# Optimization experiments

Hardware: AMD Instinct MI355X
Metric: run time of the kernel (lower is better)

Reference implementation:

```python
import jax, jax.numpy as jnp
import numpy as np
from functools import partial

B, S, D_IN, H = 8, 2048, 1024, 1024
V = 50257
NUM_CODEWORDS, EMB_DIM = 256, 16
NUM_NEURONS, TOP_K = 64, 16  # top_k = sparsity(0.25) * 64
TILE_ROWS = 16
NUM_TILES = H // TILE_ROWS  # 64 -> decoder out_features = 1024
FREQS = (1.0, 2.0, 4.0)
MAX_LEN = 1024


def setup_inputs() -> dict:
    key = jax.random.key(0)
    ks = jax.random.split(key, 16)
    s = 0.02
    return {
        "inputs": jax.random.normal(ks[0], (B, S, D_IN), jnp.float32),
        "Wt": jax.random.normal(ks[1], (H, D_IN), jnp.float32) * s,
        "bt": jnp.zeros((H,), jnp.float32),
        "Wq": jax.random.normal(ks[2], (H, H), jnp.float32) * s,
        "bq": jnp.zeros((H,), jnp.float32),
        "Wk": jax.random.normal(ks[3], (H, H), jnp.float32) * s,
        "bk": jnp.zeros((H,), jnp.float32),
        "Wv": jax.random.normal(ks[4], (H, H), jnp.float32) * s,
        "bv": jnp.zeros((H,), jnp.float32),
        "Wo": jax.random.normal(ks[5], (D_IN, H), jnp.float32) * s,
        "bo": jnp.zeros((D_IN,), jnp.float32),
        "codebook": jax.random.normal(ks[6], (NUM_CODEWORDS, EMB_DIM), jnp.float32) * s,
        "instructions": jax.random.randint(ks[7], (NUM_TILES * TILE_ROWS, D_IN // EMB_DIM), 0, NUM_CODEWORDS),
        "W_lm": jax.random.normal(ks[8], (V, NUM_TILES * TILE_ROWS), jnp.float32) * s,
        "b_lm": jnp.zeros((V,), jnp.float32),
    }


def _positional_bias(seq_len):
    # AttentionBasisSynthesizer: sin/cos atoms at freqs (1,2,4), gains=1, shifts=0
    ang = 2.0 * jnp.pi * jnp.arange(seq_len, dtype=jnp.float32) / MAX_LEN
    bias = jnp.zeros((seq_len,), jnp.float32)
    for f in FREQS:
        bias = bias + jnp.sin(f * ang) + jnp.cos(f * ang)
    return bias  # [S]


def _forward(inputs, Wt, bt, Wq, bq, Wk, bk, Wv, bv, Wo, bo, codebook, instructions, W_lm, b_lm):
    tokens = inputs @ Wt.T + bt                       # [B,S,H]
    q = tokens @ Wq.T + bq
    k = tokens @ Wk.T + bk
    v = tokens @ Wv.T + bv
    # per-step KV-cache loop == causal attention over prefix; vectorize
    scores = jnp.einsum("bqh,bkh->bqk", q, k) / jnp.sqrt(jnp.float32(H))
    scores = scores + _positional_bias(S)[None, None, :]
    i = jnp.arange(S)
    causal = i[:, None] >= i[None, :]                 # [S,S]
    scores = jnp.where(causal[None], scores, -jnp.inf)
    attn = jnp.einsum("bqk,bkh->bqh", jax.nn.softmax(scores, axis=-1), v)  # [B,S,H]
    # sparse routing: group into NUM_NEURONS neurons, keep top-k by L2 norm,
    # softmax weights over kept neurons, straight-through combine with dense path
    g = attn.reshape(B, S, NUM_NEURONS, H // NUM_NEURONS)
    sc = jnp.sqrt(jnp.sum(g * g, axis=-1))            # [B,S,N]
    vals, idx = jax.lax.top_k(sc, TOP_K)              # [B,S,K]
    w = jax.nn.softmax(vals, axis=-1)
    onehot = jax.nn.one_hot(idx, NUM_NEURONS, dtype=attn.dtype)  # [B,S,K,N]
    wfull = jnp.einsum("bsk,bskn->bsn", w, onehot)    # [B,S,N]
    combined = (g * wfull[..., None]).reshape(B, S, H)
    combined = combined + (attn - jax.lax.stop_gradient(attn))  # straight-through
    dec_in = combined @ Wo.T + bo                     # [B,S,D_IN]
    x = jnp.mean(dec_in, axis=1)                      # [B,D_IN]
    # DemopackDecoder: weight rows assembled from codebook via instruction indices
    W_dec = codebook[instructions].reshape(NUM_TILES * TILE_ROWS, D_IN)
    hidden = x @ W_dec.T                              # [B, 1024]
    return hidden @ W_lm.T + b_lm                     # [B, V]


def reference(inputs, Wt, bt, Wq, bq, Wk, bk, Wv, bv, Wo, bo, codebook, instructions, W_lm, b_lm):
    return _forward(inputs, Wt, bt, Wq, bq, Wk, bk, Wv, bv, Wo, bo, codebook, instructions, W_lm, b_lm)
```

## Files before the change

### kernel.cpp

```cpp
#include <hip/hip_runtime.h>
#include <cstdint>
#include <cstddef>

#define B_   8
#define S_   2048
#define DIN_ 1024
#define H_   1024
#define V_   50257

typedef unsigned short ushort_t;
typedef __bf16 bf16x8 __attribute__((ext_vector_type(8)));
typedef float  f32x4  __attribute__((ext_vector_type(4)));

__device__ __forceinline__ ushort_t f2bf(float x) {
    unsigned u = __float_as_uint(x);
    u = (u + 0x7fffu + ((u >> 16) & 1u)) >> 16;
    return (ushort_t)u;
}

__device__ __forceinline__ void async16(const void* g, void* s) {
    __builtin_amdgcn_global_load_lds(
        (const __attribute__((address_space(1))) unsigned int*)g,
        (__attribute__((address_space(3))) unsigned int*)s, 16, 0, 0);
}

__device__ __forceinline__ float wredmax(float v) {
#pragma unroll
    for (int o = 32; o; o >>= 1) v = fmaxf(v, __shfl_xor(v, o));
    return v;
}
__device__ __forceinline__ float wredsum(float v) {
#pragma unroll
    for (int o = 32; o; o >>= 1) v += __shfl_xor(v, o);
    return v;
}

__global__ void f2bf_vec(const float* __restrict__ in, ushort_t* __restrict__ out, int n4) {
    int i = blockIdx.x * 256 + threadIdx.x;
    if (i >= n4) return;
    float4 f = ((const float4*)in)[i];
    ushort4 u;
    u.x = f2bf(f.x); u.y = f2bf(f.y); u.z = f2bf(f.z); u.w = f2bf(f.w);
    ((ushort4*)out)[i] = u;
}

__global__ void f2bf_w3(const float* __restrict__ Wq, const float* __restrict__ Wk,
                        const float* __restrict__ Wv, ushort_t* __restrict__ out) {
    int i = blockIdx.x * 256 + threadIdx.x;
    int w = i >> 18, off = i & 262143;
    const float* src = w == 0 ? Wq : (w == 1 ? Wk : Wv);
    float4 f = ((const float4*)src)[off];
    ushort4 u;
    u.x = f2bf(f.x); u.y = f2bf(f.y); u.z = f2bf(f.z); u.w = f2bf(f.w);
    ((ushort4*)(out + (size_t)w * 1048576))[off] = u;
}

__global__ void pos_bias_kernel(float* __restrict__ bias) {
    int k = blockIdx.x * 256 + threadIdx.x;
    if (k >= S_) return;
    float ang = 6.283185307179586f * (float)k / 1024.0f;
    float b = 0.f;
    b += sinf(1.f * ang) + cosf(1.f * ang);
    b += sinf(2.f * ang) + cosf(2.f * ang);
    b += sinf(4.f * ang) + cosf(4.f * ang);
    bias[k] = b;
}

__global__ __launch_bounds__(256)
void transpose_wt(const float* __restrict__ Wt, ushort_t* __restrict__ wtT) {
    __shared__ float t[64][65];
    int k0 = blockIdx.x * 64, i0 = blockIdx.y * 64;
    int tx = threadIdx.x & 63, ty = threadIdx.x >> 6;
#pragma unroll
    for (int j = 0; j < 16; j++) {
        int k = ty * 16 + j;
        t[k][tx] = Wt[(size_t)(k0 + k) * DIN_ + i0 + tx];
    }
    __syncthreads();
#pragma unroll
    for (int j = 0; j < 16; j++) {
        int i = ty * 16 + j;
        wtT[(size_t)(i0 + i) * H_ + k0 + tx] = f2bf(t[tx][i]);
    }
}

__global__ __launch_bounds__(256)
void bcomb_kernel(const float* __restrict__ Wq, const float* __restrict__ Wk,
                  const float* __restrict__ Wv, const float* __restrict__ bq,
                  const float* __restrict__ bk, const float* __restrict__ bv,
                  const float* __restrict__ bt, float* __restrict__ bcomb) {
    int wave = threadIdx.x >> 6, lane = threadIdx.x & 63;
    int j = blockIdx.x * 4 + wave;
    const float* W  = j < 1024 ? Wq : (j < 2048 ? Wk : Wv);
    const float* bb = j < 1024 ? bq : (j < 2048 ? bk : bv);
    int rowj = j & 1023;
    const float4* wr4 = (const float4*)(W + (size_t)rowj * 1024);
    const float4* bt4 = (const float4*)bt;
    float s = 0.f;
#pragma unroll
    for (int c = 0; c < 4; c++) {
        float4 w = wr4[c * 64 + lane];
        float4 b = bt4[c * 64 + lane];
        s += w.x * b.x + w.y * b.y + w.z * b.z + w.w * b.w;
    }
    s = wredsum(s);
    if (lane == 0) bcomb[j] = s + bb[rowj];
}

template <int OUT_BF16>
__global__ __launch_bounds__(256)
void gemm_bt(const ushort_t* __restrict__ A, int lda,
             const ushort_t* __restrict__ Bt, int ldb,
             void* __restrict__ Cv, int ldc, int K, const float* __restrict__ bias) {
    int bn = blockIdx.x, bm = blockIdx.y;
    __shared__ ushort_t As[128 * 32];
    __shared__ ushort_t Bs[128 * 32];
    int tid = threadIdx.x, wave = tid >> 6, lane = tid & 63;
    int wr = wave >> 1, wc = wave & 1;
    int nkt = K >> 5;
    int srow = lane >> 2, scol = (lane & 3) * 8;
    size_t arow0 = (size_t)bm * 128, brow0 = (size_t)bn * 128;
    f32x4 acc[4][4];
#pragma unroll
    for (int m = 0; m < 4; m++)
#pragma unroll
        for (int n = 0; n < 4; n++) acc[m][n] = f32x4{0.f, 0.f, 0.f, 0.f};
    for (int kt = 0; kt < nkt; ++kt) {
        int k0 = kt * 32;
#pragma unroll
        for (int i = 0; i < 2; i++) {
            int reg = wave * 2 + i;
            int row = reg * 16 + srow;
            async16(A + (arow0 + row) * (size_t)lda + k0 + scol, (ushort_t*)As + reg * 512);
            async16(Bt + (brow0 + row) * (size_t)ldb + k0 + scol, (ushort_t*)Bs + reg * 512);
        }
        __syncthreads();
        bf16x8 af[4], bfr[4];
#pragma unroll
        for (int m = 0; m < 4; m++)
            af[m] = *(const bf16x8*)&As[(wr * 64 + m * 16 + (lane & 15)) * 32 + (lane >> 4) * 8];
#pragma unroll
        for (int n = 0; n < 4; n++)
            bfr[n] = *(const bf16x8*)&Bs[(wc * 64 + n * 16 + (lane & 15)) * 32 + (lane >> 4) * 8];
#pragma unroll
        for (int m = 0; m < 4; m++)
#pragma unroll
            for (int n = 0; n < 4; n++)
                acc[m][n] = __builtin_amdgcn_mfma_f32_16x16x32_bf16(af[m], bfr[n], acc[m][n], 0, 0, 0);
        __syncthreads();
    }
    int rl = (lane >> 4) * 4, cl = lane & 15;
#pragma unroll
    for (int m = 0; m < 4; m++)
#pragma unroll
        for (int n = 0; n < 4; n++) {
            int col = bn * 128 + wc * 64 + n * 16 + cl;
            float badd = bias ? bias[col] : 0.f;
#pragma unroll
            for (int r = 0; r < 4; r++) {
                int row = bm * 128 + wr * 64 + m * 16 + rl + r;
                float v = acc[m][n][r] + badd;
                size_t off = (size_t)row * ldc + col;
                if (OUT_BF16) ((ushort_t*)Cv)[off] = f2bf(v);
                else          ((float*)Cv)[off] = v;
            }
        }
}

template <int OUT_BF16, int MODE>
__global__ __launch_bounds__(512, 2)
void gemm256(const ushort_t* __restrict__ A, size_t sAb, int lda,
             const ushort_t* __restrict__ Bt, size_t sBb, int ldb,
             void* __restrict__ Cv, size_t sCb, int ldc,
             int K, const float* __restrict__ bias, int nbn, int nwg,
             float* __restrict__ Cv2) {
    extern __shared__ char lds[];
    int bz = blockIdx.y;
    int bm, bn, koff = 0, nkt;
    void* Cuse = Cv;
    size_t sCuse = sCb;
    if (MODE == 2) {
        int x = blockIdx.x;
        if (x < 32) {
            bm = x >> 2; bn = x & 3;
            int km = (bm + 1) * 256; if (km > 1024) km = 1024;
            nkt = km >> 6;
        } else {
            int j = x - 32;
            bm = 7 - (j >> 2); bn = j & 3;
            koff = 1024;
            nkt = ((bm + 1) * 256 - 1024) >> 6;
            Cuse = Cv2;
            sCuse = (size_t)1024 * 1024;
        }
    } else {
        int orig = blockIdx.x;
        int qq = nwg >> 3, rr8 = nwg & 7;
        int xcd = orig & 7, bidx = orig >> 3;
        int wgid = (xcd < rr8 ? xcd * (qq + 1) : rr8 * (qq + 1) + (xcd - rr8) * qq) + bidx;
        if (MODE == 1) {
            int w = wgid;
            bm = 0;
            while ((bm + 1) * (bm + 2) / 2 <= w) bm++;
            bn = w - bm * (bm + 1) / 2;
        } else {
            bm = wgid / nbn; bn = wgid - bm * nbn;
        }
        nkt = K >> 6;
    }

    const ushort_t* Ab = A + (size_t)bz * sAb;
    const ushort_t* Bb = Bt + (size_t)bz * sBb;
    int tid = threadIdx.x, wave = tid >> 6, lane = tid & 63;
    int wr = wave >> 2, wc = wave & 3;

    int srow = wave * 8 + (lane >> 3);
    int sswz = ((lane & 7) ^ (lane >> 3)) * 8;
    const ushort_t* Ag = Ab + ((size_t)bm * 256 + srow) * (size_t)lda + sswz + koff;
    const ushort_t* Bg = Bb + ((size_t)bn * 256 + srow) * (size_t)ldb + sswz + koff;
    int sdst = wave * 1024;

    int fr = lane & 15, g = lane >> 4;
    int kx = (fr >> 2) & 1;
    int gsw = (g ^ (fr & 3)) * 16;
    int aoff = wr * 16384 + fr * 128 + gsw;
    int boff = 32768 + (wc >> 1) * 16384 + ((wc & 1) * 64 + fr) * 128 + gsw;
    int ks0 = kx << 6, ks1 = (kx ^ 1) << 6;

    f32x4 acc[8][4];
#pragma unroll
    for (int m = 0; m < 8; m++)
#pragma unroll
        for (int n = 0; n < 4; n++) acc[m][n] = f32x4{0.f, 0.f, 0.f, 0.f};

#define STG_A(t, h, bo)                                                        \
    do {                                                                       \
        async16(Ag + (size_t)((h) * 128) * lda + (t) * 64,                     \
                lds + (bo) + (h) * 16384 + sdst);                              \
        async16(Ag + (size_t)((h) * 128 + 64) * lda + (t) * 64,                \
                lds + (bo) + (h) * 16384 + 8192 + sdst);                       \
    } while (0)
#define STG_B(t, h, bo)                                                        \
    do {                                                                       \
        async16(Bg + (size_t)((h) * 128) * ldb + (t) * 64,                     \
                lds + (bo) + 32768 + (h) * 16384 + sdst);                      \
        async16(Bg + (size_t)((h) * 128 + 64) * ldb + (t) * 64,                \
                lds + (bo) + 32768 + (h) * 16384 + 8192 + sdst);               \
    } while (0)

    STG_A(0, 0, 0); STG_A(0, 1, 0); STG_B(0, 0, 0); STG_B(0, 1, 0);
    STG_A(1, 0, 65536); STG_A(1, 1, 65536); STG_B(1, 0, 65536); STG_B(1, 1, 65536);
    asm volatile("s_waitcnt vmcnt(8)" ::: "memory");
    __builtin_amdgcn_sched_barrier(0);
    __builtin_amdgcn_s_barrier();
    __builtin_amdgcn_sched_barrier(0);

    bf16x8 af03[4][2], af47[4][2], bf01[2][2], bf23[2][2];
#pragma unroll
    for (int mf = 0; mf < 4; mf++) {
        af03[mf][0] = *(const bf16x8*)(lds + aoff + mf * 2048 + ks0);
        af03[mf][1] = *(const bf16x8*)(lds + aoff + mf * 2048 + ks1);
    }
#pragma unroll
    for (int nf = 0; nf < 2; nf++) {
        bf01[nf][0] = *(const bf16x8*)(lds + boff + nf * 2048 + ks0);
        bf01[nf][1] = *(const bf16x8*)(lds + boff + nf * 2048 + ks1);
    }

    int bufo = 0;
    for (int t = 0; t < nkt; ++t, bufo ^= 65536) {
        int nb = bufo ^ 65536;
#pragma unroll
        for (int mf = 0; mf < 4; mf++) {
            af47[mf][0] = *(const bf16x8*)(lds + bufo + aoff + (mf + 4) * 2048 + ks0);
            af47[mf][1] = *(const bf16x8*)(lds + bufo + aoff + (mf + 4) * 2048 + ks1);
        }
        __builtin_amdgcn_s_setprio(1);
#pragma unroll
        for (int mf = 0; mf < 4; mf++)
#pragma unroll
            for (int nf = 0; nf < 2; nf++) {
                acc[mf][nf] = __builtin_amdgcn_mfma_f32_16x16x32_bf16(af03[mf][0], bf01[nf][0], acc[mf][nf], 0, 0, 0);
                acc[mf][nf] = __builtin_amdgcn_mfma_f32_16x16x32_bf16(af03[mf][1], bf01[nf][1], acc[mf][nf], 0, 0, 0);
            }
        __builtin_amdgcn_s_setprio(0);
        __builtin_amdgcn_sched_barrier(0);
        asm volatile("s_waitcnt lgkmcnt(0)" ::: "memory");
        __builtin_amdgcn_sched_barrier(0);
        __builtin_amdgcn_s_barrier();
        __builtin_amdgcn_sched_barrier(0);

#pragma unroll
        for (int nf = 0; nf < 2; nf++) {
            bf23[nf][0] = *(const bf16x8*)(lds + bufo + boff + (nf + 2) * 2048 + ks0);
            bf23[nf][1] = *(const bf16x8*)(lds + bufo + boff + (nf + 2) * 2048 + ks1);
        }
        __builtin_amdgcn_s_setprio(1);
#pragma unroll
        for (int mf = 0; mf < 4; mf++)
#pragma unroll
            for (int nf = 0; nf < 2; nf++) {
                acc[mf + 4][nf] = __builtin_amdgcn_mfma_f32_16x16x32_bf16(af47[mf][0], bf01[nf][0], acc[mf + 4][nf], 0, 0, 0);
                acc[mf + 4][nf] = __builtin_amdgcn_mfma_f32_16x16x32_bf16(af47[mf][1], bf01[nf][1], acc[mf + 4][nf], 0, 0, 0);
            }
        __builtin_amdgcn_s_setprio(0);
        __builtin_amdgcn_sched_barrier(0);
        __builtin_amdgcn_s_barrier();
        __builtin_amdgcn_sched_barrier(0);

        if (t + 2 < nkt) STG_A(t + 2, 0, bufo);
        __builtin_amdgcn_s_setprio(1);
#pragma unroll
        for (int mf = 0; mf < 4; mf++)
#pragma unroll
            for (int nf = 0; nf < 2; nf++) {
                acc[mf][nf + 2] = __builtin_amdgcn_mfma_f32_16x16x32_bf16(af03[mf][0], bf23[nf][0], acc[mf][nf + 2], 0, 0, 0);
                acc[mf][nf + 2] = __builtin_amdgcn_mfma_f32_16x16x32_bf16(af03[mf][1], bf23[nf][1], acc[mf][nf + 2], 0, 0, 0);
            }
        __builtin_amdgcn_s_setprio(0);
        __builtin_amdgcn_sched_barrier(0);
        if (t + 1 < nkt) {
            if (t + 2 < nkt) { asm volatile("s_waitcnt vmcnt(2)" ::: "memory"); }
            else             { asm volatile("s_waitcnt vmcnt(0)" ::: "memory"); }
        }
        __builtin_amdgcn_s_barrier();
        __builtin_amdgcn_sched_barrier(0);

        if (t + 1 < nkt) {
#pragma unroll
            for (int mf = 0; mf < 4; mf++) {
                af03[mf][0] = *(const bf16x8*)(lds + nb + aoff + mf * 2048 + ks0);
                af03[mf][1] = *(const bf16x8*)(lds + nb + aoff + mf * 2048 + ks1);
            }
#pragma unroll
            for (int nf = 0; nf < 2; nf++) {
                bf01[nf][0] = *(const bf16x8*)(lds + nb + boff + nf * 2048 + ks0);
                bf01[nf][1] = *(const bf16x8*)(lds + nb + boff + nf * 2048 + ks1);
            }
        }
        if (t + 2 < nkt) { STG_A(t + 2, 1, bufo); STG_B(t + 2, 0, bufo); STG_B(t + 2, 1, bufo); }
        __builtin_amdgcn_s_setprio(1);
#pragma unroll
        for (int mf = 0; mf < 4; mf++)
#pragma unroll
            for (int nf = 0; nf < 2; nf++) {
                acc[mf + 4][nf + 2] = __builtin_amdgcn_mfma_f32_16x16x32_bf16(af47[mf][0], bf23[nf][0], acc[mf + 4][nf + 2], 0, 0, 0);
                acc[mf + 4][nf + 2] = __builtin_amdgcn_mfma_f32_16x16x32_bf16(af47[mf][1], bf23[nf][1], acc[mf + 4][nf + 2], 0, 0, 0);
            }
        __builtin_amdgcn_s_setprio(0);
        __builtin_amdgcn_sched_barrier(0);
        __builtin_amdgcn_s_barrier();
        __builtin_amdgcn_sched_barrier(0);
    }
#undef STG_A
#undef STG_B

    int rl = (lane >> 4) * 4, cl = lane & 15;
#pragma unroll
    for (int mf = 0; mf < 8; mf++)
#pragma unroll
        for (int nf = 0; nf < 4; nf++) {
            int col = bn * 256 + wc * 64 + nf * 16 + cl;
            float badd = bias ? bias[col] : 0.f;
#pragma unroll
            for (int r = 0; r < 4; r++) {
                int row = bm * 256 + wr * 128 + mf * 16 + rl + r;
                float v = acc[mf][nf][r] + badd;
                size_t off = (size_t)bz * sCuse + (size_t)row * ldc + col;
                if (OUT_BF16) ((ushort_t*)Cuse)[off] = f2bf(v);
                else          ((float*)Cuse)[off] = v;
            }
        }
}

__global__ __launch_bounds__(256)
void transpose_v(const ushort_t* __restrict__ qkv, ushort_t* __restrict__ vT) {
    __shared__ ushort_t t[64][66];
    int b = blockIdx.z;
    int s0 = blockIdx.x * 64, h0 = blockIdx.y * 64;
    int tx = threadIdx.x & 63, ty = threadIdx.x >> 6;
#pragma unroll
    for (int i = 0; i < 16; i++) {
        int s = ty * 16 + i;
        t[s][tx] = qkv[((size_t)b * S_ + s0 + s) * 3072 + 2048 + h0 + tx];
    }
    __syncthreads();
#pragma unroll
    for (int i = 0; i < 16; i++) {
        int h = ty * 16 + i;
        vT[((size_t)b * H_ + h0 + h) * S_ + s0 + tx] = t[tx][h];
    }
}

__global__ __launch_bounds__(256)
void softmax_kernel(const float* __restrict__ scores, ushort_t* __restrict__ P,
                    const float* __restrict__ bias) {
    __shared__ float red[8];
    int q = blockIdx.x, b = blockIdx.y;
    int L = q + 1;
    int tid = threadIdx.x;
    const float4* srow4 = (const float4*)(scores + ((size_t)b * S_ + q) * S_);
    const float4* bias4 = (const float4*)bias;
    const float scale = 0.03125f;
    int kz = ((q >> 8) + 1) * 256;

    int k00 = tid * 4, k01 = 1024 + tid * 4;
    float4 v0 = {0.f, 0.f, 0.f, 0.f}, v1 = {0.f, 0.f, 0.f, 0.f};
    float lm = -3e38f;
    if (k00 < kz) {
        float4 s4 = srow4[tid];
        float4 b4 = bias4[tid];
        v0.x = (k00 + 0 < L) ? s4.x * scale + b4.x : -3e38f;
        v0.y = (k00 + 1 < L) ? s4.y * scale + b4.y : -3e38f;
        v0.z = (k00 + 2 < L) ? s4.z * scale + b4.z : -3e38f;
        v0.w = (k00 + 3 < L) ? s4.w * scale + b4.w : -3e38f;
        lm = fmaxf(fmaxf(v0.x, v0.y), fmaxf(v0.z, v0.w));
    }
    if (k01 < kz) {
        float4 s4 = srow4[256 + tid];
        float4 b4 = bias4[256 + tid];
        v1.x = (k01 + 0 < L) ? s4.x * scale + b4.x : -3e38f;
        v1.y = (k01 + 1 < L) ? s4.y * scale + b4.y : -3e38f;
        v1.z = (k01 + 2 < L) ? s4.z * scale + b4.z : -3e38f;
        v1.w = (k01 + 3 < L) ? s4.w * scale + b4.w : -3e38f;
        lm = fmaxf(lm, fmaxf(fmaxf(v1.x, v1.y), fmaxf(v1.z, v1.w)));
    }
    lm = wredmax(lm);
    if ((tid & 63) == 0) red[tid >> 6] = lm;
    __syncthreads();
    float m = fmaxf(fmaxf(red[0], red[1]), fmaxf(red[2], red[3]));

    float ls = 0.f;
    if (k00 < kz) {
        v0.x = __expf(v0.x - m); v0.y = __expf(v0.y - m);
        v0.z = __expf(v0.z - m); v0.w = __expf(v0.w - m);
        ls += v0.x + v0.y + v0.z + v0.w;
    }
    if (k01 < kz) {
        v1.x = __expf(v1.x - m); v1.y = __expf(v1.y - m);
        v1.z = __expf(v1.z - m); v1.w = __expf(v1.w - m);
        ls += v1.x + v1.y + v1.z + v1.w;
    }
    ls = wredsum(ls);
    if ((tid & 63) == 0) red[4 + (tid >> 6)] = ls;
    __syncthreads();
    float invs = 1.f / (red[4] + red[5] + red[6] + red[7]);

    ushort_t* prow = P + ((size_t)b * S_ + q) * S_;
    if (k00 < kz) {
        ushort4 o;
        o.x = f2bf(v0.x * invs); o.y = f2bf(v0.y * invs);
        o.z = f2bf(v0.z * invs); o.w = f2bf(v0.w * invs);
        ((ushort4*)prow)[tid] = o;
    }
    if (k01 < kz) {
        ushort4 o;
        o.x = f2bf(v1.x * invs); o.y = f2bf(v1.y * invs);
        o.z = f2bf(v1.z * invs); o.w = f2bf(v1.w * invs);
        ((ushort4*)prow)[256 + tid] = o;
    }
}

__global__ __launch_bounds__(256)
void routing_kernel(const float* __restrict__ attn, const float* __restrict__ attn2,
                    ushort_t* __restrict__ combined) {
    int wave = threadIdx.x >> 6, lane = threadIdx.x & 63;
    size_t row = (size_t)blockIdx.x * 4 + wave;
    const float4* a4 = (const float4*)(attn + row * H_);
    float4 x0 = a4[lane * 4 + 0], x1 = a4[lane * 4 + 1];
    float4 x2 = a4[lane * 4 + 2], x3 = a4[lane * 4 + 3];
    int q = (int)(row & 2047);
    if (q >= 1024) {
        size_t b = row >> 11;
        const float4* a2 = (const float4*)(attn2 + ((b * 1024 + (size_t)(q - 1024)) * H_));
        float4 y0 = a2[lane * 4 + 0], y1 = a2[lane * 4 + 1];
        float4 y2 = a2[lane * 4 + 2], y3 = a2[lane * 4 + 3];
        x0.x += y0.x; x0.y += y0.y; x0.z += y0.z; x0.w += y0.w;
        x1.x += y1.x; x1.y += y1.y; x1.z += y1.z; x1.w += y1.w;
        x2.x += y2.x; x2.y += y2.y; x2.z += y2.z; x2.w += y2.w;
        x3.x += y3.x; x3.y += y3.y; x3.z += y3.z; x3.w += y3.w;
    }
    float ss = x0.x * x0.x + x0.y * x0.y + x0.z * x0.z + x0.w * x0.w
             + x1.x * x1.x + x1.y * x1.y + x1.z * x1.z + x1.w * x1.w
             + x2.x * x2.x + x2.y * x2.y + x2.z * x2.z + x2.w * x2.w
             + x3.x * x3.x + x3.y * x3.y + x3.z * x3.z + x3.w * x3.w;
    float sc = sqrtf(ss);

    float v = sc, thr = 0.f, mx = 0.f;
#pragma unroll
    for (int i = 0; i < 16; i++) {
        float mm = wredmax(v);
        if (i == 0) mx = mm;
        thr = mm;
        if (v == mm) v = -1e30f;
    }
    float e = (sc >= thr) ? __expf(sc - mx) : 0.f;
    float se = wredsum(e);
    float w = e / se;

    const float xs[16] = {x0.x, x0.y, x0.z, x0.w, x1.x, x1.y, x1.z, x1.w,
                          x2.x, x2.y, x2.z, x2.w, x3.x, x3.y, x3.z, x3.w};
    union { ushort_t u[16]; uint4 q4[2]; } pk;
#pragma unroll
    for (int j = 0; j < 16; j++) pk.u[j] = f2bf(xs[j] * w);
    uint4* dst = (uint4*)(combined + row * H_ + lane * 16);
    dst[0] = pk.q4[0];
    dst[1] = pk.q4[1];
}

__global__ void cmean_part(const ushort_t* __restrict__ comb, float* __restrict__ part) {
    int d = blockIdx.x * 256 + threadIdx.x;
    int sc = blockIdx.y, b = blockIdx.z;
    const ushort_t* p = comb + ((size_t)b * S_ + sc * 128) * H_ + d;
    float s = 0.f;
    for (int i = 0; i < 128; i++) s += __uint_as_float((unsigned)p[(size_t)i * H_] << 16);
    part[((size_t)b * 16 + sc) * H_ + d] = s;
}

__global__ void cmean_final(const float* __restrict__ part, float* __restrict__ cm) {
    int idx = blockIdx.x * 256 + threadIdx.x;
    int b = idx >> 10, d = idx & 1023;
    float s = 0.f;
#pragma unroll
    for (int c = 0; c < 16; c++) s += part[((size_t)b * 16 + c) * DIN_ + d];
    cm[idx] = s * (1.0f / 2048.0f);
}

__global__ __launch_bounds__(256)
void xgemv(const float* __restrict__ cm, const float* __restrict__ Wo,
           const float* __restrict__ bo, float* __restrict__ x) {
    int wave = threadIdx.x >> 6, lane = threadIdx.x & 63;
    int i = blockIdx.x * 4 + wave;
    const float4* wr4 = (const float4*)(Wo + (size_t)i * H_);
    float4 w[4];
#pragma unroll
    for (int c = 0; c < 4; c++) w[c] = wr4[c * 64 + lane];
    float accv[B_];
#pragma unroll
    for (int b = 0; b < B_; b++) {
        const float4* c4 = (const float4*)(cm + (size_t)b * H_);
        float s = 0.f;
#pragma unroll
        for (int c = 0; c < 4; c++) {
            float4 h = c4[c * 64 + lane];
            s += w[c].x * h.x + w[c].y * h.y + w[c].z * h.z + w[c].w * h.w;
        }
        accv[b] = wredsum(s);
    }
    if (lane == 0) {
        float bi = bo[i];
#pragma unroll
        for (int b = 0; b < B_; b++) x[(size_t)b * DIN_ + i] = accv[b] + bi;
    }
}

__global__ __launch_bounds__(64)
void decode_hidden(const float* __restrict__ x, const float* __restrict__ codebook,
                   const int* __restrict__ instr, float* __restrict__ hidden) {
    int r = blockIdx.x;
    int lane = threadIdx.x;
    int idx = instr[r * 64 + lane];
    const float4* cw = (const float4*)(codebook + (size_t)idx * 16);
    float4 c0 = cw[0], c1 = cw[1], c2 = cw[2], c3 = cw[3];
    float acc[B_];
#pragma unroll
    for (int b = 0; b < B_; b++) {
        const float4* xb = (const float4*)(x + (size_t)b * DIN_ + lane * 16);
        float4 h0 = xb[0], h1 = xb[1], h2 = xb[2], h3 = xb[3];
        acc[b] = c0.x * h0.x + c0.y * h0.y + c0.z * h0.z + c0.w * h0.w
               + c1.x * h1.x + c1.y * h1.y + c1.z * h1.z + c1.w * h1.w
               + c2.x * h2.x + c2.y * h2.y + c2.z * h2.z + c2.w * h2.w
               + c3.x * h3.x + c3.y * h3.y + c3.z * h3.z + c3.w * h3.w;
    }
#pragma unroll
    for (int b = 0; b < B_; b++) acc[b] = wredsum(acc[b]);
    if (lane == 0) {
#pragma unroll
        for (int b = 0; b < B_; b++) hidden[(size_t)b * 1024 + r] = acc[b];
    }
}

__global__ __launch_bounds__(256)
void lm_head(const float* __restrict__ Wlm, const float* __restrict__ hidden,
             const float* __restrict__ blm, float* __restrict__ out) {
    int wave = threadIdx.x >> 6, lane = threadIdx.x & 63;
    for (int v = blockIdx.x * 4 + wave; v < V_; v += gridDim.x * 4) {
        const float4* wrow = (const float4*)(Wlm + (size_t)v * 1024);
        float acc[B_];
#pragma unroll
        for (int b = 0; b < B_; b++) acc[b] = 0.f;
#pragma unroll
        for (int rr = 0; rr < 4; rr++) {
            float4 wv = wrow[rr * 64 + lane];
#pragma unroll
            for (int b = 0; b < B_; b++) {
                float4 hv = ((const float4*)hidden)[b * 256 + rr * 64 + lane];
                acc[b] += wv.x * hv.x + wv.y * hv.y + wv.z * hv.z + wv.w * hv.w;
            }
        }
#pragma unroll
        for (int b = 0; b < B_; b++) acc[b] = wredsum(acc[b]);
        if (lane == 0) {
            float bl = blm[v];
#pragma unroll
            for (int b = 0; b < B_; b++) out[(size_t)b * V_ + v] = acc[b] + bl;
        }
    }
}

extern "C" void kernel_launch(void* const* d_in, const int* in_sizes, int n_in,
                              void* d_out, int out_size, void* d_ws, size_t ws_size,
                              hipStream_t stream) {
    const float* inputs = (const float*)d_in[0];
    const float* Wt  = (const float*)d_in[1];
    const float* bt  = (const float*)d_in[2];
    const float* Wq  = (const float*)d_in[3];
    const float* bq  = (const float*)d_in[4];
    const float* Wk  = (const float*)d_in[5];
    const float* bk  = (const float*)d_in[6];
    const float* Wv  = (const float*)d_in[7];
    const float* bv  = (const float*)d_in[8];
    const float* Wo  = (const float*)d_in[9];
    const float* bo  = (const float*)d_in[10];
    const float* codebook = (const float*)d_in[11];
    const int*   instructions = (const int*)d_in[12];
    const float* Wlm = (const float*)d_in[13];
    const float* blm = (const float*)d_in[14];
    float* out = (float*)d_out;

    (void)hipFuncSetAttribute(reinterpret_cast<const void*>(&gemm256<1, 0>),
                              hipFuncAttributeMaxDynamicSharedMemorySize, 131072);
    (void)hipFuncSetAttribute(reinterpret_cast<const void*>(&gemm256<0, 1>),
                              hipFuncAttributeMaxDynamicSharedMemorySize, 131072);
    (void)hipFuncSetAttribute(reinterpret_cast<const void*>(&gemm256<0, 2>),
                              hipFuncAttributeMaxDynamicSharedMemorySize, 131072);

    const size_t MB = 1024 * 1024;
    char* ws = (char*)d_ws;
    ushort_t* wqkv_bf = (ushort_t*)(ws + 0);
    ushort_t* wtT_bf  = (ushort_t*)(ws + 6 * MB);
    ushort_t* wcomb   = (ushort_t*)(ws + 8 * MB);
    float* bcomb  = (float*)(ws + 14 * MB);
    float* pbias  = (float*)(ws + 14 * MB + 64 * 1024);
    float* cm     = (float*)(ws + 14 * MB + 128 * 1024);
    float* xbuf   = (float*)(ws + 14 * MB + 192 * 1024);
    float* hidden = (float*)(ws + 14 * MB + 256 * 1024);
    float* part   = (float*)(ws + 14 * MB + 512 * 1024);
    ushort_t* inbf   = (ushort_t*)(ws + 16 * MB);
    ushort_t* qkv    = (ushort_t*)(ws + 48 * MB);
    ushort_t* vT     = (ushort_t*)(ws + 144 * MB);
    float* scores    = (float*)(ws + 176 * MB);
    ushort_t* P      = (ushort_t*)(ws + 304 * MB);
    float* attn      = (float*)(ws + 48 * MB);
    float* attn2     = (float*)(ws + 112 * MB);
    ushort_t* combined = (ushort_t*)(ws + 176 * MB);

    f2bf_vec<<<16384, 256, 0, stream>>>(inputs, inbf, 4194304);
    f2bf_w3<<<3072, 256, 0, stream>>>(Wq, Wk, Wv, wqkv_bf);
    transpose_wt<<<dim3(16, 16), 256, 0, stream>>>(Wt, wtT_bf);
    bcomb_kernel<<<768, 256, 0, stream>>>(Wq, Wk, Wv, bq, bk, bv, bt, bcomb);
    pos_bias_kernel<<<8, 256, 0, stream>>>(pbias);

    gemm_bt<1><<<dim3(8, 24), 256, 0, stream>>>(wqkv_bf, 1024, wtT_bf, 1024,
                                                wcomb, 1024, 1024, nullptr);

    gemm256<1, 0><<<dim3(768, 1), 512, 131072, stream>>>(
        inbf, 0, 1024, wcomb, 0, 1024, qkv, 0, 3072, 1024, bcomb, 12, 768, nullptr);

    transpose_v<<<dim3(32, 16, 8), 256, 0, stream>>>(qkv, vT);

    gemm256<0, 1><<<dim3(36, 8), 512, 131072, stream>>>(
        qkv, (size_t)S_ * 3072, 3072, qkv + 1024, (size_t)S_ * 3072, 3072,
        scores, (size_t)S_ * S_, S_, 1024, nullptr, 36, 36, nullptr);

    softmax_kernel<<<dim3(S_, B_), 256, 0, stream>>>(scores, P, pbias);

    gemm256<0, 2><<<dim3(48, 8), 512, 131072, stream>>>(
        P, (size_t)S_ * S_, S_, vT, (size_t)H_ * S_, S_,
        attn, (size_t)S_ * H_, H_, S_, nullptr, 0, 0, attn2 - (size_t)1024 * 1024);

    routing_kernel<<<4096, 256, 0, stream>>>(attn, attn2, combined);

    cmean_part<<<dim3(4, 16, 8), 256, 0, stream>>>(combined, part);
    cmean_final<<<32, 256, 0, stream>>>(part, cm);
    xgemv<<<256, 256, 0, stream>>>(cm, Wo, bo, xbuf);

    decode_hidden<<<1024, 64, 0, stream>>>(xbuf, codebook, instructions, hidden);

    lm_head<<<2048, 256, 0, stream>>>(Wlm, hidden, blm, out);
}
```

Baseline: 451.5 us.

## Merge setup kernels into one launch and fold V transpose into QK^T GEMM

Five small preprocessing kernels (bf16 conversions, Wt transpose, combined bias, positional bias) are merged into a single block-range-dispatched kernel to cut launch overhead. The separate V-transpose kernel is removed. Its work now runs in extra workgroups (64 per batch) appended to the QK^T scores GEMM grid, so the transpose overlaps with the GEMM tiles. The extra blocks reuse the GEMM's large LDS allocation and 512-thread shape, which may hurt occupancy or scheduling of the GEMM tiles.

```diff
diff --git a/kernel.cpp b/kernel.cpp
--- a/kernel.cpp
+++ b/kernel.cpp
@@ -35,76 +35,77 @@
     return v;
 }
 
-__global__ void f2bf_vec(const float* __restrict__ in, ushort_t* __restrict__ out, int n4) {
-    int i = blockIdx.x * 256 + threadIdx.x;
-    if (i >= n4) return;
-    float4 f = ((const float4*)in)[i];
-    ushort4 u;
-    u.x = f2bf(f.x); u.y = f2bf(f.y); u.z = f2bf(f.z); u.w = f2bf(f.w);
-    ((ushort4*)out)[i] = u;
-}
-
-__global__ void f2bf_w3(const float* __restrict__ Wq, const float* __restrict__ Wk,
-                        const float* __restrict__ Wv, ushort_t* __restrict__ out) {
-    int i = blockIdx.x * 256 + threadIdx.x;
-    int w = i >> 18, off = i & 262143;
-    const float* src = w == 0 ? Wq : (w == 1 ? Wk : Wv);
-    float4 f = ((const float4*)src)[off];
-    ushort4 u;
-    u.x = f2bf(f.x); u.y = f2bf(f.y); u.z = f2bf(f.z); u.w = f2bf(f.w);
-    ((ushort4*)(out + (size_t)w * 1048576))[off] = u;
-}
-
-__global__ void pos_bias_kernel(float* __restrict__ bias) {
-    int k = blockIdx.x * 256 + threadIdx.x;
-    if (k >= S_) return;
-    float ang = 6.283185307179586f * (float)k / 1024.0f;
-    float b = 0.f;
-    b += sinf(1.f * ang) + cosf(1.f * ang);
-    b += sinf(2.f * ang) + cosf(2.f * ang);
-    b += sinf(4.f * ang) + cosf(4.f * ang);
-    bias[k] = b;
-}
-
+#define NB0 16384
+#define NB1 19456
+#define NB2 19712
+#define NB3 20480
+#define NB4 20488
 __global__ __launch_bounds__(256)
-void transpose_wt(const float* __restrict__ Wt, ushort_t* __restrict__ wtT) {
-    __shared__ float t[64][65];
-    int k0 = blockIdx.x * 64, i0 = blockIdx.y * 64;
-    int tx = threadIdx.x & 63, ty = threadIdx.x >> 6;
-#pragma unroll
-    for (int j = 0; j < 16; j++) {
-        int k = ty * 16 + j;
-        t[k][tx] = Wt[(size_t)(k0 + k) * DIN_ + i0 + tx];
-    }
-    __syncthreads();
-#pragma unroll
-    for (int j = 0; j < 16; j++) {
-        int i = ty * 16 + j;
-        wtT[(size_t)(i0 + i) * H_ + k0 + tx] = f2bf(t[tx][i]);
-    }
-}
-
-__global__ __launch_bounds__(256)
-void bcomb_kernel(const float* __restrict__ Wq, const float* __restrict__ Wk,
-                  const float* __restrict__ Wv, const float* __restrict__ bq,
-                  const float* __restrict__ bk, const float* __restrict__ bv,
-                  const float* __restrict__ bt, float* __restrict__ bcomb) {
-    int wave = threadIdx.x >> 6, lane = threadIdx.x & 63;
-    int j = blockIdx.x * 4 + wave;
-    const float* W  = j < 1024 ? Wq : (j < 2048 ? Wk : Wv);
-    const float* bb = j < 1024 ? bq : (j < 2048 ? bk : bv);
-    int rowj = j & 1023;
-    const float4* wr4 = (const float4*)(W + (size_t)rowj * 1024);
-    const float4* bt4 = (const float4*)bt;
-    float s = 0.f;
-#pragma unroll
-    for (int c = 0; c < 4; c++) {
-        float4 w = wr4[c * 64 + lane];
-        float4 b = bt4[c * 64 + lane];
-        s += w.x * b.x + w.y * b.y + w.z * b.z + w.w * b.w;
-    }
-    s = wredsum(s);
-    if (lane == 0) bcomb[j] = s + bb[rowj];
+void setup_all(const float* __restrict__ inputs,
+               const float* __restrict__ Wq, const float* __restrict__ Wk,
+               const float* __restrict__ Wv, const float* __restrict__ Wt,
+               const float* __restrict__ bq, const float* __restrict__ bk,
+               const float* __restrict__ bv, const float* __restrict__ bt,
+               ushort_t* __restrict__ inbf, ushort_t* __restrict__ wqkv_bf,
+               ushort_t* __restrict__ wtT, float* __restrict__ bcomb,
+               float* __restrict__ pbias) {
+    __shared__ float twt[64][65];
+    int blk = blockIdx.x, tid = threadIdx.x;
+    if (blk < NB0) {
+        int i = blk * 256 + tid;
+        float4 f = ((const float4*)inputs)[i];
+        ushort4 u;
+        u.x = f2bf(f.x); u.y = f2bf(f.y); u.z = f2bf(f.z); u.w = f2bf(f.w);
+        ((ushort4*)inbf)[i] = u;
+    } else if (blk < NB1) {
+        int i = (blk - NB0) * 256 + tid;
+        int w = i >> 18, off = i & 262143;
+        const float* src = w == 0 ? Wq : (w == 1 ? Wk : Wv);
+        float4 f = ((const float4*)src)[off];
+        ushort4 u;
+        u.x = f2bf(f.x); u.y = f2bf(f.y); u.z = f2bf(f.z); u.w = f2bf(f.w);
+        ((ushort4*)(wqkv_bf + (size_t)w * 1048576))[off] = u;
+    } else if (blk < NB2) {
+        int j = blk - NB1;
+        int k0 = (j & 15) * 64, i0 = (j >> 4) * 64;
+        int tx = tid & 63, ty = tid >> 6;
+#pragma unroll
+        for (int jj = 0; jj < 16; jj++) {
+            int k = ty * 16 + jj;
+            twt[k][tx] = Wt[(size_t)(k0 + k) * DIN_ + i0 + tx];
+        }
+        __syncthreads();
+#pragma unroll
+        for (int jj = 0; jj < 16; jj++) {
+            int i = ty * 16 + jj;
+            wtT[(size_t)(i0 + i) * H_ + k0 + tx] = f2bf(twt[tx][i]);
+        }
+    } else if (blk < NB3) {
+        int wave = tid >> 6, lane = tid & 63;
+        int j = (blk - NB2) * 4 + wave;
+        const float* W  = j < 1024 ? Wq : (j < 2048 ? Wk : Wv);
+        const float* bb = j < 1024 ? bq : (j < 2048 ? bk : bv);
+        int rowj = j & 1023;
+        const float4* wr4 = (const float4*)(W + (size_t)rowj * 1024);
+        const float4* bt4 = (const float4*)bt;
+        float s = 0.f;
+#pragma unroll
+        for (int c = 0; c < 4; c++) {
+            float4 w = wr4[c * 64 + lane];
+            float4 b = bt4[c * 64 + lane];
+            s += w.x * b.x + w.y * b.y + w.z * b.z + w.w * b.w;
+        }
+        s = wredsum(s);
+        if (lane == 0) bcomb[j] = s + bb[rowj];
+    } else {
+        int k = (blk - NB3) * 256 + tid;
+        float ang = 6.283185307179586f * (float)k / 1024.0f;
+        float b = 0.f;
+        b += sinf(1.f * ang) + cosf(1.f * ang);
+        b += sinf(2.f * ang) + cosf(2.f * ang);
+        b += sinf(4.f * ang) + cosf(4.f * ang);
+        pbias[k] = b;
+    }
 }
 
 template <int OUT_BF16>
@@ -193,19 +194,46 @@
             Cuse = Cv2;
             sCuse = (size_t)1024 * 1024;
         }
+    } else if (MODE == 1) {
+        int orig = blockIdx.x;
+        if (orig >= 36) {
+            ushort_t (*t)[66] = (ushort_t(*)[66])lds;
+            ushort_t* vT = (ushort_t*)Cv2;
+            const ushort_t* qkvp = A;
+            int j = orig - 36;
+            int tx = threadIdx.x & 63, ty = threadIdx.x >> 6;
+            for (int rep = 0; rep < 8; rep++) {
+                int tile = j * 8 + rep;
+                int s0 = (tile & 31) * 64, h0 = (tile >> 5) * 64;
+#pragma unroll
+                for (int i = 0; i < 8; i++) {
+                    int s = ty * 8 + i;
+                    t[s][tx] = qkvp[((size_t)bz * S_ + s0 + s) * 3072 + 2048 + h0 + tx];
+                }
+                __syncthreads();
+#pragma unroll
+                for (int i = 0; i < 8; i++) {
+                    int h = ty * 8 + i;
+                    vT[((size_t)bz * H_ + h0 + h) * S_ + s0 + tx] = t[tx][h];
+                }
+                __syncthreads();
+            }
+            return;
+        }
+        int qq = 36 >> 3, rr8 = 36 & 7;
+        int xcd = orig & 7, bidx = orig >> 3;
+        int wgid = (xcd < rr8 ? xcd * (qq + 1) : rr8 * (qq + 1) + (xcd - rr8) * qq) + bidx;
+        int w = wgid;
+        bm = 0;
+        while ((bm + 1) * (bm + 2) / 2 <= w) bm++;
+        bn = w - bm * (bm + 1) / 2;
+        nkt = K >> 6;
     } else {
         int orig = blockIdx.x;
         int qq = nwg >> 3, rr8 = nwg & 7;
         int xcd = orig & 7, bidx = orig >> 3;
         int wgid = (xcd < rr8 ? xcd * (qq + 1) : rr8 * (qq + 1) + (xcd - rr8) * qq) + bidx;
-        if (MODE == 1) {
-            int w = wgid;
-            bm = 0;
-            while ((bm + 1) * (bm + 2) / 2 <= w) bm++;
-            bn = w - bm * (bm + 1) / 2;
-        } else {
-            bm = wgid / nbn; bn = wgid - bm * nbn;
-        }
+        bm = wgid / nbn; bn = wgid - bm * nbn;
         nkt = K >> 6;
     }
 
@@ -371,25 +399,6 @@
                 else          ((float*)Cuse)[off] = v;
             }
         }
-}
-
-__global__ __launch_bounds__(256)
-void transpose_v(const ushort_t* __restrict__ qkv, ushort_t* __restrict__ vT) {
-    __shared__ ushort_t t[64][66];
-    int b = blockIdx.z;
-    int s0 = blockIdx.x * 64, h0 = blockIdx.y * 64;
-    int tx = threadIdx.x & 63, ty = threadIdx.x >> 6;
-#pragma unroll
-    for (int i = 0; i < 16; i++) {
-        int s = ty * 16 + i;
-        t[s][tx] = qkv[((size_t)b * S_ + s0 + s) * 3072 + 2048 + h0 + tx];
-    }
-    __syncthreads();
-#pragma unroll
-    for (int i = 0; i < 16; i++) {
-        int h = ty * 16 + i;
-        vT[((size_t)b * H_ + h0 + h) * S_ + s0 + tx] = t[tx][h];
-    }
 }
 
 __global__ __launch_bounds__(256)
@@ -655,11 +664,8 @@
     float* attn2     = (float*)(ws + 112 * MB);
     ushort_t* combined = (ushort_t*)(ws + 176 * MB);
 
-    f2bf_vec<<<16384, 256, 0, stream>>>(inputs, inbf, 4194304);
-    f2bf_w3<<<3072, 256, 0, stream>>>(Wq, Wk, Wv, wqkv_bf);
-    transpose_wt<<<dim3(16, 16), 256, 0, stream>>>(Wt, wtT_bf);
-    bcomb_kernel<<<768, 256, 0, stream>>>(Wq, Wk, Wv, bq, bk, bv, bt, bcomb);
-    pos_bias_kernel<<<8, 256, 0, stream>>>(pbias);
+    setup_all<<<NB4, 256, 0, stream>>>(inputs, Wq, Wk, Wv, Wt, bq, bk, bv, bt,
+                                       inbf, wqkv_bf, wtT_bf, bcomb, pbias);
 
     gemm_bt<1><<<dim3(8, 24), 256, 0, stream>>>(wqkv_bf, 1024, wtT_bf, 1024,
                                                 wcomb, 1024, 1024, nullptr);
@@ -667,11 +673,9 @@
     gemm256<1, 0><<<dim3(768, 1), 512, 131072, stream>>>(
         inbf, 0, 1024, wcomb, 0, 1024, qkv, 0, 3072, 1024, bcomb, 12, 768, nullptr);
 
-    transpose_v<<<dim3(32, 16, 8), 256, 0, stream>>>(qkv, vT);
-
-    gemm256<0, 1><<<dim3(36, 8), 512, 131072, stream>>>(
+    gemm256<0, 1><<<dim3(100, 8), 512, 131072, stream>>>(
         qkv, (size_t)S_ * 3072, 3072, qkv + 1024, (size_t)S_ * 3072, 3072,
-        scores, (size_t)S_ * S_, S_, 1024, nullptr, 36, 36, nullptr);
+        scores, (size_t)S_ * S_, S_, 1024, nullptr, 36, 36, (float*)vT);
 
     softmax_kernel<<<dim3(S_, B_), 256, 0, stream>>>(scores, P, pbias);
 
```

Result: faster. 433.5 us (-4.0%).
